# Performance work log

Hardware: AMD Instinct MI355X
Metric: run time of the kernel (lower is better)

The kernel has to match this reference:

```python
import jax, jax.numpy as jnp
import numpy as np

B, L, H, D, TXT = 128, 512, 336, 256, 768
K, S, EMB = 16, 4, 128
H_SCALE = 0.15
EPS, ITERS = 0.05, 30
ALPHA, BETA = 1.0, 0.5
GW, TAU = 0.5, 0.07
LMB_MSE, LMB_COT, LMB_DELTA, LMB_ENT, LMB_TV = 1.0, 0.1, 0.1, 0.01, 0.01


def setup_inputs() -> dict:
    key = jax.random.key(0)
    ks = jax.random.split(key, 12)
    def xav(k, shape):
        return jax.random.normal(k, shape, jnp.float32) / np.sqrt(shape[0]).astype(np.float32)
    inp = {}
    inp['y_res'] = jax.random.normal(ks[0], (B, H, D), jnp.float32)
    inp['text_emb'] = jax.random.normal(ks[1], (B, TXT), jnp.float32)
    inp['enc_out'] = jax.random.normal(ks[2], (B, L, D), jnp.float32)
    inp['y_future'] = jax.random.normal(ks[3], (B, H, D), jnp.float32)
    inp['perm'] = jax.random.permutation(ks[4], EMB)
    inp['W_t2k'] = xav(ks[5], (TXT, K * (3 + S))); inp['b_t2k'] = jnp.zeros((K * (3 + S),), jnp.float32)
    inp['W_kemb'] = xav(ks[6], (H, EMB)); inp['b_kemb'] = jnp.zeros((EMB,), jnp.float32)
    inp['W_tir'] = xav(ks[7], (1, D)); inp['b_tir'] = jnp.zeros((D,), jnp.float32)
    inp['var_proj'] = jnp.ones((D,), jnp.float32)
    inp['W_g1'] = xav(ks[8], (2 * D + TXT, 512)); inp['b_g1'] = jnp.zeros((512,), jnp.float32)
    inp['W_g2'] = xav(ks[9], (512, D)); inp['b_g2'] = jnp.zeros((D,), jnp.float32)
    inp['W_fp'] = xav(ks[10], (3 * D, EMB)); inp['b_fp'] = jnp.zeros((EMB,), jnp.float32)
    return inp


def _text2kernels(text_emb, W, b):
    # text -> K temporal kernels: mixture of S shape bases with learned mu/sigma/amp
    raw = (text_emb @ W + b).reshape(-1, K, 3 + S)
    mu = jax.nn.sigmoid(raw[..., 0])                       # [B,K] center in [0,1]
    sig = jax.nn.softplus(raw[..., 1]) * H_SCALE + 1e-3     # [B,K] width
    amp = jax.nn.softplus(raw[..., 2])                      # [B,K]
    shape_w = jax.nn.softmax(raw[..., 3:], axis=-1)         # [B,K,S]
    t = (jnp.arange(H, dtype=text_emb.dtype) + 0.5) / H     # [H]
    z = (t[None, None, :] - mu[..., None]) / sig[..., None]  # [B,K,H]
    az = jnp.abs(z)
    in_supp = (az <= 1.0).astype(z.dtype)
    basis = jnp.stack([
        jnp.exp(-0.5 * z * z),
        jnp.exp(-az),
        jnp.maximum(1.0 - az, 0.0),
        0.5 * (1.0 + jnp.cos(jnp.pi * jnp.clip(z, -1.0, 1.0))) * in_supp,
    ], axis=-1)                                             # [B,K,H,S]
    kappa = amp[..., None] * jnp.einsum('bkhs,bks->bkh', basis, shape_w)
    return kappa, mu, shape_w


def _future_proj(y, W, b):
    # concat(y, first diff, second diff) -> linear, in_dim = 3*D
    d1 = jnp.diff(y, axis=1, prepend=y[:, :1])
    d2 = jnp.diff(d1, axis=1, prepend=d1[:, :1])
    return jnp.concatenate([y, d1, d2], axis=-1) @ W + b    # [B,H,EMB]


def _l2n(x):
    return x / (jnp.linalg.norm(x, axis=-1, keepdims=True) + 1e-8)


def _causal_cost(k_emb, f_pos, mu):
    cossim = jnp.einsum('bkd,bhd->bkh', _l2n(k_emb), _l2n(f_pos))
    t = (jnp.arange(H, dtype=k_emb.dtype) + 0.5) / H
    causal = jnp.maximum(mu[:, :, None] - t[None, None, :], 0.0)  # effect-before-cause penalty
    return ALPHA * (1.0 - cossim) + BETA * causal            # [B,K,H]


def _sinkhorn(C, r, c):
    Kmat = jnp.exp(-C / EPS)
    def body(i, uv):
        u, v = uv
        u = r / (jnp.einsum('bkh,bh->bk', Kmat, v) + 1e-9)
        v = c / (jnp.einsum('bkh,bk->bh', Kmat, u) + 1e-9)
        return (u, v)
    u, v = jax.lax.fori_loop(0, ITERS, body, (jnp.ones_like(r), jnp.ones_like(c)))
    return u[:, :, None] * Kmat * v[:, None, :]              # [B,K,H]


def _delta_contrastive(k_emb, f_pos, Pi, negatives):
    w = Pi / (jnp.sum(Pi, axis=-1, keepdims=True) + 1e-9)    # transport-weighted aggregation
    kn = _l2n(k_emb)
    def sim(f):
        return jnp.einsum('bkd,bkd->bk', kn, _l2n(jnp.einsum('bkh,bhd->bkd', w, f)))
    logits = jnp.stack([sim(f_pos)] + [sim(f) for f in negatives], axis=-1) / TAU  # [B,K,1+neg]
    return -jnp.mean(jax.nn.log_softmax(logits, axis=-1)[..., 0])


def reference(y_res, text_emb, enc_out, y_future, perm, W_t2k, b_t2k, W_kemb, b_kemb,
              W_tir, b_tir, var_proj, W_g1, b_g1, W_g2, b_g2, W_fp, b_fp):
    # --- text-induced response ---
    kappa, mu, shape_w = _text2kernels(text_emb, W_t2k, b_t2k)   # [B,K,H]
    y_tir_scalar = kappa.sum(axis=1)                             # [B,H]
    # --- gated fusion ---
    y_tir = (y_tir_scalar[..., None] @ W_tir + b_tir) * var_proj[None, None, :]  # [B,H,D]
    ts_global = enc_out.mean(axis=1)                             # [B,D]
    gate_in = jnp.concatenate([ts_global, text_emb, jnp.broadcast_to(var_proj[None, :], (y_res.shape[0], D))], axis=-1)
    gate = jax.nn.sigmoid(jax.nn.relu(gate_in @ W_g1 + b_g1) @ W_g2 + b_g2)[:, None, :]  # [B,1,D]
    y_hat = y_res + GW * gate * (y_tir - y_res)
    # --- aux losses ---
    k_emb = kappa @ W_kemb + b_kemb                              # [B,K,EMB]
    f_pos = _future_proj(y_future, W_fp, b_fp)                   # [B,H,EMB]
    C = _causal_cost(k_emb, f_pos, mu)
    r = jax.lax.stop_gradient(kappa.sum(-1) + 1e-6)
    r = r / r.sum(axis=-1, keepdims=True)
    c = jnp.full((C.shape[0], C.shape[2]), 1.0 / C.shape[2], C.dtype)
    Pi = _sinkhorn(C, r, c)
    shift = max(1, H // 6)
    f_neg1 = jnp.roll(f_pos, shift, axis=1)
    f_neg2 = f_pos[..., perm]
    loss_delta = _delta_contrastive(k_emb, f_pos, Pi, [f_neg1, f_neg2])
    loss_cot = jnp.mean(jnp.sum(C * Pi, axis=(1, 2)))
    sw = jnp.maximum(shape_w, 1e-8)
    loss_ent = -jnp.mean(jnp.sum(sw * jnp.log(sw), axis=-1))
    loss_tv = jnp.mean(jnp.abs(mu[:, 1:] - mu[:, :-1]))
    loss_mse = jnp.mean((y_hat - y_future) ** 2)
    return (LMB_MSE * loss_mse + LMB_COT * loss_cot + LMB_DELTA * loss_delta
            + LMB_ENT * loss_ent + LMB_TV * loss_tv)
```

## Files before the change

### kernel.cpp

```cpp
#include <hip/hip_runtime.h>
#include <math.h>

#define Bn   128
#define Ln   512
#define Hn   336
#define Dn   256
#define TXTn 768
#define Kn   16
#define EMBn 128
#define SHIFT 56
#define MSEB 1024
#define FROWS 48
#define FTILES 7
#define ASTRIDE 776

typedef __attribute__((ext_vector_type(8))) short short8;
typedef __attribute__((ext_vector_type(4))) float floatx4;

__device__ __forceinline__ float softplusf(float x){
  return fmaxf(x, 0.f) + log1pf(expf(-fabsf(x)));
}
__device__ __forceinline__ unsigned short f2bf(float x){
  unsigned int u = __float_as_uint(x);
  unsigned int r = (u + 0x7fffu + ((u >> 16) & 1u)) >> 16;
  return (unsigned short)r;
}
__device__ __forceinline__ float rcpf(float x){ return __builtin_amdgcn_rcpf(x); }
__device__ __forceinline__ float wsum(float x){
  x += __shfl_xor(x, 1);  x += __shfl_xor(x, 2);  x += __shfl_xor(x, 4);
  x += __shfl_xor(x, 8);  x += __shfl_xor(x, 16); x += __shfl_xor(x, 32);
  return x;
}

__global__ __launch_bounds__(256) void k_fused1(
    const float* __restrict__ text, const float* __restrict__ W, const float* __restrict__ bb,
    float* __restrict__ mu_o, float* __restrict__ kapT, float* __restrict__ rr_o,
    float* __restrict__ ytirs, float* __restrict__ part_ent, float* __restrict__ part_tv){
  int b = blockIdx.x, t = threadIdx.x;
  __shared__ float kapS[Kn*Hn];
  __shared__ float musL[Kn], sigL[Kn], ampL[Kn], shwL[Kn*4], entS[Kn], rrS[Kn];
  __shared__ float red[256];
  __shared__ float comb[112];
  __shared__ float totS;
  {
    int o = t & 127, half = t >> 7;
    if (o < 112){
      const float* tb = text + (size_t)b*TXTn + half*384;
      const float* Wb = W + (size_t)half*384*112 + o;
      float a0=0.f, a1=0.f, a2=0.f, a3=0.f;
      for (int i = 0; i < 384; i += 4){
        float4 x = *(const float4*)(tb + i);
        a0 += x.x*Wb[(i+0)*112]; a1 += x.y*Wb[(i+1)*112];
        a2 += x.z*Wb[(i+2)*112]; a3 += x.w*Wb[(i+3)*112];
      }
      red[half*112 + o] = (a0 + a1) + (a2 + a3);
    }
  }
  __syncthreads();
  if (t < 112) comb[t] = red[t] + red[112 + t] + bb[t];
  __syncthreads();
  if (t < Kn){
    float r0 = comb[t*7+0], r1 = comb[t*7+1], r2 = comb[t*7+2];
    float mu  = 1.f/(1.f+expf(-r0));
    float sig = softplusf(r1)*0.15f + 1e-3f;
    float amp = softplusf(r2);
    float s0 = comb[t*7+3], s1 = comb[t*7+4], s2 = comb[t*7+5], s3 = comb[t*7+6];
    float m = fmaxf(fmaxf(s0,s1), fmaxf(s2,s3));
    float e0 = expf(s0-m), e1 = expf(s1-m), e2 = expf(s2-m), e3 = expf(s3-m);
    float inv = 1.f/(e0+e1+e2+e3);
    float w0 = e0*inv, w1 = e1*inv, w2 = e2*inv, w3 = e3*inv;
    musL[t] = mu; sigL[t] = sig; ampL[t] = amp;
    shwL[t*4+0] = w0; shwL[t*4+1] = w1; shwL[t*4+2] = w2; shwL[t*4+3] = w3;
    mu_o[b*Kn + t] = mu;
    float ent = 0.f, sw;
    sw = fmaxf(w0,1e-8f); ent += sw*logf(sw);
    sw = fmaxf(w1,1e-8f); ent += sw*logf(sw);
    sw = fmaxf(w2,1e-8f); ent += sw*logf(sw);
    sw = fmaxf(w3,1e-8f); ent += sw*logf(sw);
    entS[t] = ent;
  }
  __syncthreads();
  for (int p = t; p < Kn*Hn; p += 256){
    int k = p/Hn, h = p - k*Hn;
    float mu = musL[k], sig = sigL[k], amp = ampL[k];
    float w0 = shwL[k*4+0], w1 = shwL[k*4+1], w2 = shwL[k*4+2], w3 = shwL[k*4+3];
    float tt = (h + 0.5f)/(float)Hn;
    float z  = (tt - mu)/sig;
    float az = fabsf(z);
    float b0 = expf(-0.5f*z*z);
    float b1 = expf(-az);
    float b2 = fmaxf(1.f-az, 0.f);
    float zc = fminf(fmaxf(z,-1.f),1.f);
    float b3 = (az <= 1.f) ? 0.5f*(1.f+cosf(3.14159265358979f*zc)) : 0.f;
    kapS[p] = amp*(w0*b0 + w1*b1 + w2*b2 + w3*b3);
  }
  __syncthreads();
  for (int q = t; q < Kn*Hn; q += 256){
    int h = q >> 4, k = q & 15;
    kapT[((size_t)b*Hn + h)*Kn + k] = kapS[k*Hn + h];
  }
  {
    int k = t >> 4, j16 = t & 15;
    float s = 0.f;
    for (int h = j16; h < Hn; h += 16) s += kapS[k*Hn + h];
    red[t] = s;
  }
  __syncthreads();
  if (t < Kn){
    float s = 0.f;
    for (int j = 0; j < 16; ++j) s += red[t*16 + j];
    rrS[t] = s + 1e-6f;
  }
  __syncthreads();
  if (t == 0){
    float tot = 0.f, tv = 0.f, es = 0.f;
    for (int k = 0; k < Kn; ++k) tot += rrS[k];
    for (int k = 1; k < Kn; ++k) tv += fabsf(musL[k]-musL[k-1]);
    for (int k = 0; k < Kn; ++k) es += entS[k];
    totS = tot; part_tv[b] = tv; part_ent[b] = es;
  }
  __syncthreads();
  if (t < Kn) rr_o[b*Kn + t] = rrS[t]/totS;
  for (int h = t; h < Hn; h += 256){
    float s = 0.f;
    #pragma unroll
    for (int k = 0; k < Kn; ++k) s += kapS[k*Hn + h];
    ytirs[b*Hn + h] = s;
  }
}

__global__ __launch_bounds__(128) void k_kemb1(const float* __restrict__ kapT,
    const float* __restrict__ W, float* __restrict__ kp){
  int blk = blockIdx.x;
  int b = blk >> 3, oc = blk & 7;
  int e = threadIdx.x;
  float acc[Kn];
  #pragma unroll
  for (int k = 0; k < Kn; ++k) acc[k] = 0.f;
  const float* kb = kapT + (size_t)b*Hn*Kn;
  int h0 = oc*42, h1 = h0 + 42;
  for (int h = h0; h < h1; ++h){
    float wv = W[h*EMBn + e];
    const float4* kr = (const float4*)(kb + h*Kn);
    float4 c0 = kr[0], c1 = kr[1], c2 = kr[2], c3 = kr[3];
    acc[0]  += c0.x*wv; acc[1]  += c0.y*wv; acc[2]  += c0.z*wv; acc[3]  += c0.w*wv;
    acc[4]  += c1.x*wv; acc[5]  += c1.y*wv; acc[6]  += c1.z*wv; acc[7]  += c1.w*wv;
    acc[8]  += c2.x*wv; acc[9]  += c2.y*wv; acc[10] += c2.z*wv; acc[11] += c2.w*wv;
    acc[12] += c3.x*wv; acc[13] += c3.y*wv; acc[14] += c3.z*wv; acc[15] += c3.w*wv;
  }
  float* kpb = kp + ((size_t)blk*Kn)*EMBn + e;
  #pragma unroll
  for (int k = 0; k < Kn; ++k) kpb[(size_t)k*EMBn] = acc[k];
}

__global__ __launch_bounds__(256) void k_kemb2(const float* __restrict__ kp,
    const float* __restrict__ bb, float* __restrict__ kn_o){
  int b = blockIdx.x, t = threadIdx.x;
  __shared__ float kS[Kn*EMBn];
  __shared__ float r2[256];
  __shared__ float invS[Kn];
  for (int j = t; j < Kn*EMBn; j += 256){
    int e = j & 127;
    float s = bb[e];
    const float* p = kp + (size_t)b*8*Kn*EMBn + j;
    #pragma unroll
    for (int oc = 0; oc < 8; ++oc) s += p[(size_t)oc*Kn*EMBn];
    kS[j] = s;
  }
  __syncthreads();
  {
    int k = t & 15, g = t >> 4;
    float s = 0.f;
    for (int e = g; e < EMBn; e += 16){ float v = kS[k*EMBn + e]; s += v*v; }
    r2[g*Kn + k] = s;
  }
  __syncthreads();
  if (t < Kn){
    float s = 0.f;
    for (int g = 0; g < 16; ++g) s += r2[g*Kn + t];
    invS[t] = 1.f/(sqrtf(s) + 1e-8f);
  }
  __syncthreads();
  for (int j = t; j < Kn*EMBn; j += 256)
    kn_o[(size_t)b*Kn*EMBn + j] = kS[j]*invS[j >> 7];
}

__global__ void k_wprep(const float* __restrict__ W, unsigned short* __restrict__ Bsw){
  int tid = blockIdx.x*256 + threadIdx.x;
  int k = tid >> 7, n = tid & 127;
  int kt = k >> 5, kr = k & 31, quad = kr >> 3, j = kr & 7;
  int c = n >> 4, ln = n & 15;
  int lane = quad*16 + ln;
  int dst = ((kt*8 + c)*64 + lane)*8 + j;
  Bsw[dst] = f2bf(W[k*128 + n]);
}

__global__ __launch_bounds__(256) void k_encmean(const float* __restrict__ enc,
                                                 float* __restrict__ psum){
  int blk = blockIdx.x;
  int b = blk >> 3, p = blk & 7;
  int t = threadIdx.x;
  int d4 = t & 63, rg = t >> 6;
  const float4* e4 = (const float4*)(enc + (size_t)b*Ln*Dn);
  float4 s = make_float4(0.f,0.f,0.f,0.f);
  for (int l = p + 8*rg; l < Ln; l += 32){
    float4 v = e4[(size_t)l*64 + d4];
    s.x += v.x; s.y += v.y; s.z += v.z; s.w += v.w;
  }
  __shared__ float4 red[256];
  red[t] = s;
  __syncthreads();
  if (rg == 0){
    float4 o = red[d4];
    #pragma unroll
    for (int r = 1; r < 4; ++r){
      float4 v = red[r*64 + d4];
      o.x += v.x; o.y += v.y; o.z += v.z; o.w += v.w;
    }
    ((float4*)(psum + ((size_t)b*8 + p)*Dn))[d4] = o;
  }
}

__global__ __launch_bounds__(256) void k_gmlp1(const float* __restrict__ psum,
    const float* __restrict__ text, const float* __restrict__ vp,
    const float* __restrict__ W1, float* __restrict__ hidp){
  int bt = blockIdx.x >> 5, hc = (blockIdx.x >> 2) & 7, ks = blockIdx.x & 3;
  int t = threadIdx.x;
  __shared__ float inS[4][320];
  for (int j = t; j < 4*320; j += 256){
    int bi = j / 320, jj = j - bi*320;
    int gi = ks*320 + jj;
    int b = bt*4 + bi;
    float vsl;
    if (gi < Dn){
      float s = 0.f;
      for (int p = 0; p < 8; ++p) s += psum[((size_t)b*8 + p)*Dn + gi];
      vsl = s * (1.f/(float)Ln);
    } else if (gi < Dn + TXTn){
      vsl = text[(size_t)b*TXTn + (gi - Dn)];
    } else {
      vsl = vp[gi - Dn - TXTn];
    }
    inS[bi][jj] = vsl;
  }
  __syncthreads();
  int h = t & 63, bi = t >> 6;
  int hidx = hc*64 + h;
  const float* Wb = W1 + (size_t)(ks*320)*512 + hidx;
  float a0 = 0.f, a1 = 0.f, a2 = 0.f, a3 = 0.f;
  const float4* in4 = (const float4*)inS[bi];
  for (int i = 0; i < 320; i += 4){
    float4 x = in4[i >> 2];
    a0 += x.x*Wb[(size_t)(i+0)*512]; a1 += x.y*Wb[(size_t)(i+1)*512];
    a2 += x.z*Wb[(size_t)(i+2)*512]; a3 += x.w*Wb[(size_t)(i+3)*512];
  }
  hidp[((size_t)ks*Bn + bt*4 + bi)*512 + hidx] = (a0 + a1) + (a2 + a3);
}

__global__ __launch_bounds__(256) void k_gmlp2(const float* __restrict__ hidp,
    const float* __restrict__ b1, const float* __restrict__ W2,
    const float* __restrict__ b2, float* __restrict__ gate_o){
  int bt = blockIdx.x >> 3, dc = blockIdx.x & 7;
  int t = threadIdx.x;
  __shared__ float hS[4][512];
  __shared__ float pS[8][4][32];
  for (int j = t; j < 4*512; j += 256){
    int bi = j >> 9, i = j & 511;
    size_t bidx = (size_t)(bt*4 + bi)*512 + i;
    float s = hidp[bidx] + hidp[(size_t)Bn*512 + bidx]
            + hidp[(size_t)2*Bn*512 + bidx] + hidp[(size_t)3*Bn*512 + bidx];
    hS[bi][i] = fmaxf(s + b1[i], 0.f);
  }
  __syncthreads();
  {
    int dl = t & 31, ig = t >> 5;
    int d  = dc*32 + dl;
    float a0=0.f, a1=0.f, a2=0.f, a3=0.f;
    int i0 = ig*64;
    for (int i = i0; i < i0 + 64; ++i){
      float wv = W2[(size_t)i*Dn + d];
      a0 += hS[0][i]*wv; a1 += hS[1][i]*wv;
      a2 += hS[2][i]*wv; a3 += hS[3][i]*wv;
    }
    pS[ig][0][dl] = a0; pS[ig][1][dl] = a1;
    pS[ig][2][dl] = a2; pS[ig][3][dl] = a3;
  }
  __syncthreads();
  if (t < 128){
    int bi = t >> 5, dl = t & 31;
    float s = 0.f;
    #pragma unroll
    for (int g = 0; g < 8; ++g) s += pS[g][bi][dl];
    s += b2[dc*32 + dl];
    gate_o[(size_t)(bt*4 + bi)*Dn + dc*32 + dl] = 1.f/(1.f + expf(-s));
  }
}

__global__ __launch_bounds__(256) void k_fposm(const float* __restrict__ yf,
    const unsigned short* __restrict__ Bsw, const float* __restrict__ bb,
    float* __restrict__ fpos, float* __restrict__ finv){
  int b = blockIdx.x / FTILES, tile = blockIdx.x % FTILES;
  int t = threadIdx.x;
  int h0 = tile*FROWS;
  __shared__ unsigned short yS[FROWS*ASTRIDE];
  __shared__ float rsq[4][FROWS];
  const float* yb = yf + (size_t)b*Hn*Dn;

  #pragma unroll
  for (int u = 0; u < 12; ++u){
    int unit = t + 256*u;
    int r = unit >> 6, d4 = unit & 63;
    int h = h0 + r;
    int hm1 = h-1 < 0 ? 0 : h-1;
    int hm2 = h-2 < 0 ? 0 : h-2;
    float4 y   = *(const float4*)(yb + (size_t)h  *Dn + d4*4);
    float4 ym1 = *(const float4*)(yb + (size_t)hm1*Dn + d4*4);
    float4 ym2 = *(const float4*)(yb + (size_t)hm2*Dn + d4*4);
    float4 d1 = make_float4(y.x-ym1.x, y.y-ym1.y, y.z-ym1.z, y.w-ym1.w);
    float4 d2 = make_float4(y.x-2.f*ym1.x+ym2.x, y.y-2.f*ym1.y+ym2.y,
                            y.z-2.f*ym1.z+ym2.z, y.w-2.f*ym1.w+ym2.w);
    union { unsigned short u16[4]; uint2 v; } p;
    unsigned short* base = &yS[r*ASTRIDE + d4*4];
    p.u16[0]=f2bf(y.x);  p.u16[1]=f2bf(y.y);  p.u16[2]=f2bf(y.z);  p.u16[3]=f2bf(y.w);
    *(uint2*)(base)        = p.v;
    p.u16[0]=f2bf(d1.x); p.u16[1]=f2bf(d1.y); p.u16[2]=f2bf(d1.z); p.u16[3]=f2bf(d1.w);
    *(uint2*)(base + 256)  = p.v;
    p.u16[0]=f2bf(d2.x); p.u16[1]=f2bf(d2.y); p.u16[2]=f2bf(d2.z); p.u16[3]=f2bf(d2.w);
    *(uint2*)(base + 512)  = p.v;
  }
  __syncthreads();

  int wv   = __builtin_amdgcn_readfirstlane(t >> 6);
  int lane = t & 63, quad = lane >> 4, ln = lane & 15;
  int c0 = wv*2;
  floatx4 acc[3][2];
  #pragma unroll
  for (int i = 0; i < 3; ++i){
    acc[i][0] = (floatx4){0.f,0.f,0.f,0.f};
    acc[i][1] = (floatx4){0.f,0.f,0.f,0.f};
  }
  #pragma unroll
  for (int kt = 0; kt < 24; ++kt){
    int aoff = kt*32 + quad*8;
    short8 a0 = *(const short8*)&yS[( 0 + ln)*ASTRIDE + aoff];
    short8 a1 = *(const short8*)&yS[(16 + ln)*ASTRIDE + aoff];
    short8 a2 = *(const short8*)&yS[(32 + ln)*ASTRIDE + aoff];
    short8 b0 = *(const short8*)&Bsw[((kt*8 + c0  )*64 + lane)*8];
    short8 b1 = *(const short8*)&Bsw[((kt*8 + c0+1)*64 + lane)*8];
    acc[0][0] = __builtin_amdgcn_mfma_f32_16x16x32_bf16(a0, b0, acc[0][0], 0, 0, 0);
    acc[0][1] = __builtin_amdgcn_mfma_f32_16x16x32_bf16(a0, b1, acc[0][1], 0, 0, 0);
    acc[1][0] = __builtin_amdgcn_mfma_f32_16x16x32_bf16(a1, b0, acc[1][0], 0, 0, 0);
    acc[1][1] = __builtin_amdgcn_mfma_f32_16x16x32_bf16(a1, b1, acc[1][1], 0, 0, 0);
    acc[2][0] = __builtin_amdgcn_mfma_f32_16x16x32_bf16(a2, b0, acc[2][0], 0, 0, 0);
    acc[2][1] = __builtin_amdgcn_mfma_f32_16x16x32_bf16(a2, b1, acc[2][1], 0, 0, 0);
  }

  float bias0 = bb[c0*16 + ln], bias1 = bb[(c0+1)*16 + ln];
  #pragma unroll
  for (int rt = 0; rt < 3; ++rt){
    #pragma unroll
    for (int reg = 0; reg < 4; ++reg){
      int lrow = rt*16 + quad*4 + reg;
      size_t row = (size_t)b*Hn + h0 + lrow;
      float v0 = acc[rt][0][reg] + bias0;
      float v1 = acc[rt][1][reg] + bias1;
      fpos[row*EMBn + c0*16 + ln]     = v0;
      fpos[row*EMBn + (c0+1)*16 + ln] = v1;
      float sq = v0*v0 + v1*v1;
      sq += __shfl_xor(sq, 1); sq += __shfl_xor(sq, 2);
      sq += __shfl_xor(sq, 4); sq += __shfl_xor(sq, 8);
      if (ln == 0) rsq[wv][lrow] = sq;
    }
  }
  __syncthreads();
  if (t < FROWS){
    float s = rsq[0][t] + rsq[1][t] + rsq[2][t] + rsq[3][t];
    finv[(size_t)b*Hn + h0 + t] = 1.f/(sqrtf(s) + 1e-8f);
  }
}

__global__ void k_mse(const float* __restrict__ yres, const float* __restrict__ yfut,
                      const float* __restrict__ gate, const float* __restrict__ ytirs,
                      const float* __restrict__ Wt, const float* __restrict__ bt,
                      const float* __restrict__ vp, float* __restrict__ part_mse){
  const long long total = (long long)Bn*Hn*Dn;
  long long tid = blockIdx.x*(long long)blockDim.x + threadIdx.x;
  long long nth = gridDim.x*(long long)blockDim.x;
  float part = 0.f;
  for (long long i4 = tid; i4*4 < total; i4 += nth){
    long long base = i4*4;
    int b = (int)(base/((long long)Hn*Dn));
    int rem = (int)(base - (long long)b*Hn*Dn);
    int h = rem/Dn, d = rem - h*Dn;
    float4 yr = *(const float4*)(yres + base);
    float4 yv = *(const float4*)(yfut + base);
    float4 g  = *(const float4*)(gate + (size_t)b*Dn + d);
    float4 wt = *(const float4*)(Wt + d);
    float4 bv = *(const float4*)(bt + d);
    float4 vv = *(const float4*)(vp + d);
    float ys = ytirs[b*Hn + h];
    float yt, yh, e;
    yt = (ys*wt.x + bv.x)*vv.x; yh = yr.x + 0.5f*g.x*(yt-yr.x); e = yh-yv.x; part += e*e;
    yt = (ys*wt.y + bv.y)*vv.y; yh = yr.y + 0.5f*g.y*(yt-yr.y); e = yh-yv.y; part += e*e;
    yt = (ys*wt.z + bv.z)*vv.z; yh = yr.z + 0.5f*g.z*(yt-yr.z); e = yh-yv.z; part += e*e;
    yt = (ys*wt.w + bv.w)*vv.w; yh = yr.w + 0.5f*g.w*(yt-yr.w); e = yh-yv.w; part += e*e;
  }
  __shared__ float red[256];
  red[threadIdx.x] = part; __syncthreads();
  for (int s = 128; s > 0; s >>= 1){
    if (threadIdx.x < s) red[threadIdx.x] += red[threadIdx.x + s];
    __syncthreads();
  }
  if (threadIdx.x == 0) part_mse[blockIdx.x] = red[0];
}

__global__ __launch_bounds__(256) void k_cost(const float* __restrict__ kn,
    const float* __restrict__ fpos, const float* __restrict__ finv,
    const float* __restrict__ mu_i, float* __restrict__ Km_g){
  int b = blockIdx.x >> 2, q = blockIdx.x & 3;
  int t = threadIdx.x;
  __shared__ float knS[Kn*132];
  __shared__ float musS[Kn];
  for (int j = t; j < Kn*EMBn; j += 256){
    int k = j >> 7, e = j & 127;
    knS[k*132 + e] = kn[(size_t)b*Kn*EMBn + j];
  }
  if (t < Kn) musS[t] = mu_i[b*Kn + t];
  __syncthreads();
  const int H0 = q*84;
  for (int p = t; p < Kn*84; p += 256){
    int k = p & 15, h = H0 + (p >> 4);
    const float4* f4 = (const float4*)(fpos + ((size_t)b*Hn + h)*EMBn);
    const float4* k4 = (const float4*)(knS + k*132);
    float s = 0.f;
    #pragma unroll 8
    for (int i = 0; i < EMBn/4; ++i){
      float4 a = k4[i], f = f4[i];
      s += a.x*f.x + a.y*f.y + a.z*f.z + a.w*f.w;
    }
    float cs = s*finv[b*Hn + h];
    float th = (h + 0.5f)/(float)Hn;
    float c  = (1.f - cs) + 0.5f*fmaxf(musS[k] - th, 0.f);
    Km_g[(size_t)b*Kn*Hn + k*Hn + h] = expf(-20.f*c);
  }
}

__global__ __launch_bounds__(64) void k_sink1w(const float* __restrict__ rr,
    float* KmwT, float* __restrict__ part_cot){
  int b = blockIdx.x, l = threadIdx.x;
  float* Kb = KmwT + (size_t)b*Kn*Hn;
  int ks = ((l&1)<<3) | ((l&2)<<1) | ((l&4)>>1) | ((l&8)>>3);
  float km[16][6];
  #pragma unroll
  for (int m = 0; m < 16; ++m){
    const float* rowp = Kb + (size_t)(ks ^ m)*Hn;
    #pragma unroll
    for (int i = 0; i < 6; ++i){
      int h = 64*i + l;
      km[m][i] = (h < Hn) ? rowp[h] : 0.f;
    }
  }
  float rrl = rr[b*Kn + ks];
  float v[6];
  #pragma unroll
  for (int i = 0; i < 6; ++i) v[i] = 1.f;
  float w[16];
  for (int it = 0; it < 30; ++it){
    float p[16];
    #pragma unroll
    for (int m = 0; m < 16; ++m){
      float a = km[m][0]*v[0] + km[m][1]*v[1] + km[m][2]*v[2];
      float c = km[m][3]*v[3] + km[m][4]*v[4] + km[m][5]*v[5];
      p[m] = a + c;
    }
    #pragma unroll
    for (int m = 0; m < 8; ++m) p[m] += __shfl_xor(p[m+8], 1);
    #pragma unroll
    for (int m = 0; m < 4; ++m) p[m] += __shfl_xor(p[m+4], 2);
    #pragma unroll
    for (int m = 0; m < 2; ++m) p[m] += __shfl_xor(p[m+2], 4);
    p[0] += __shfl_xor(p[1], 8);
    p[0] += __shfl_xor(p[0], 16);
    p[0] += __shfl_xor(p[0], 32);
    float ul = rrl * rcpf(p[0] + 1e-9f);
    w[0] = ul;
    w[1] = __shfl_xor(w[0], 8);
    w[2] = __shfl_xor(w[0], 4); w[3] = __shfl_xor(w[1], 4);
    #pragma unroll
    for (int j = 0; j < 4; ++j) w[4+j] = __shfl_xor(w[j], 2);
    #pragma unroll
    for (int j = 0; j < 8; ++j) w[8+j] = __shfl_xor(w[j], 1);
    #pragma unroll
    for (int i = 0; i < 6; ++i){
      float s0 = 0.f, s1 = 0.f;
      #pragma unroll
      for (int m = 0; m < 8; ++m){ s0 += km[m][i]*w[m]; s1 += km[m+8][i]*w[m+8]; }
      v[i] = (1.f/(float)Hn) * rcpf(s0 + s1 + 1e-9f);
    }
  }
  float q[16];
  #pragma unroll
  for (int m = 0; m < 16; ++m){
    float a = km[m][0]*v[0] + km[m][1]*v[1] + km[m][2]*v[2];
    float c = km[m][3]*v[3] + km[m][4]*v[4] + km[m][5]*v[5];
    q[m] = a + c;
  }
  #pragma unroll
  for (int m = 0; m < 8; ++m) q[m] += __shfl_xor(q[m+8], 1);
  #pragma unroll
  for (int m = 0; m < 4; ++m) q[m] += __shfl_xor(q[m+4], 2);
  #pragma unroll
  for (int m = 0; m < 2; ++m) q[m] += __shfl_xor(q[m+2], 4);
  q[0] += __shfl_xor(q[1], 8);
  q[0] += __shfl_xor(q[0], 16);
  q[0] += __shfl_xor(q[0], 32);
  float tt[16];
  tt[0] = q[0];
  tt[1] = __shfl_xor(tt[0], 8);
  tt[2] = __shfl_xor(tt[0], 4); tt[3] = __shfl_xor(tt[1], 4);
  #pragma unroll
  for (int j = 0; j < 4; ++j) tt[4+j] = __shfl_xor(tt[j], 2);
  #pragma unroll
  for (int j = 0; j < 8; ++j) tt[8+j] = __shfl_xor(tt[j], 1);
  float cot = 0.f;
  #pragma unroll
  for (int m = 0; m < 16; ++m){
    float rsinv = rcpf(w[m]*tt[m] + 1e-9f);
    float* rowp = Kb + (size_t)(ks ^ m)*Hn;
    #pragma unroll
    for (int i = 0; i < 6; ++i){
      int h = 64*i + l;
      if (h < Hn){
        float Pi = w[m]*km[m][i]*v[i];
        cot += (-0.05f)*logf(km[m][i])*Pi;
        rowp[h] = Pi*rsinv;
      }
    }
  }
  cot = wsum(cot);
  if (l == 0) part_cot[b] = cot;
}

__global__ __launch_bounds__(256) void k_agg(const float* __restrict__ kn,
    const float* __restrict__ fpos, const float* __restrict__ wT,
    const int* __restrict__ perm, float* __restrict__ part_del4){
  int b = blockIdx.x >> 2, kg = blockIdx.x & 3;
  int t = threadIdx.x;
  __shared__ float wTl[Hn*4];
  __shared__ float apH[2][4*EMBn];
  __shared__ float a1H[2][4*EMBn];
  __shared__ int permS[EMBn];
  __shared__ float redW[4];
  if (t < EMBn) permS[t] = perm[t];
  for (int j = t; j < 4*Hn; j += 256){
    int k = j & 3, h = j >> 2;
    wTl[h*4 + k] = wT[(size_t)b*Kn*Hn + (size_t)(kg*4 + k)*Hn + h];
  }
  __syncthreads();

  {
    int e = t & 127, jh = t >> 7;
    float ap[4], a1[4];
    #pragma unroll
    for (int j = 0; j < 4; ++j){ ap[j] = 0.f; a1[j] = 0.f; }
    const float* fb = fpos + (size_t)b*Hn*EMBn + e;
    int hh0 = jh*168, hh1 = hh0 + 168;
    for (int h = hh0; h < hh1; ++h){
      float fv = fb[(size_t)h*EMBn];
      int h1 = h + SHIFT; if (h1 >= Hn) h1 -= Hn;
      float4 wA = *(const float4*)&wTl[h *4];
      float4 wB = *(const float4*)&wTl[h1*4];
      ap[0] += wA.x*fv; ap[1] += wA.y*fv; ap[2] += wA.z*fv; ap[3] += wA.w*fv;
      a1[0] += wB.x*fv; a1[1] += wB.y*fv; a1[2] += wB.z*fv; a1[3] += wB.w*fv;
    }
    #pragma unroll
    for (int j = 0; j < 4; ++j){
      apH[jh][j*EMBn + e] = ap[j];
      a1H[jh][j*EMBn + e] = a1[j];
    }
  }
  __syncthreads();
  for (int j = t; j < 4*EMBn; j += 256){
    apH[0][j] += apH[1][j];
    a1H[0][j] += a1H[1][j];
  }
  __syncthreads();

  int wave = t >> 6, lane = t & 63;
  {
    int kl = wave;
    int k  = kg*4 + kl;
    float sp = 0.f, s1 = 0.f, s2 = 0.f, np = 0.f, n1 = 0.f;
    for (int e = lane; e < EMBn; e += 64){
      float kne = kn[((size_t)b*Kn + k)*EMBn + e];
      float a  = apH[0][kl*EMBn + e];
      float c1 = a1H[0][kl*EMBn + e];
      sp += kne*a; s1 += kne*c1;
      s2 += kne*apH[0][kl*EMBn + permS[e]];
      np += a*a; n1 += c1*c1;
    }
    for (int o = 32; o; o >>= 1){
      sp += __shfl_down(sp, o); s1 += __shfl_down(s1, o); s2 += __shfl_down(s2, o);
      np += __shfl_down(np, o); n1 += __shfl_down(n1, o);
    }
    if (lane == 0){
      float ip  = 1.f/(sqrtf(np) + 1e-8f);
      float i1v = 1.f/(sqrtf(n1) + 1e-8f);
      const float ti = 1.f/0.07f;
      float l0 = sp*ip*ti, l1 = s1*i1v*ti, l2 = s2*ip*ti;
      float m = fmaxf(l0, fmaxf(l1, l2));
      float lse = m + logf(expf(l0-m) + expf(l1-m) + expf(l2-m));
      redW[wave] = lse - l0;
    }
  }
  __syncthreads();
  if (t == 0) part_del4[(size_t)b*4 + kg] = redW[0] + redW[1] + redW[2] + redW[3];
}

__global__ void k_final(const float* __restrict__ part_mse, const float* __restrict__ part_cot,
                        const float* __restrict__ part_del4, const float* __restrict__ part_ent,
                        const float* __restrict__ part_tv, float* __restrict__ out){
  int t = threadIdx.x;
  __shared__ double sred[256];
  double m = 0.0;
  for (int i = t; i < MSEB; i += 256) m += (double)part_mse[i];
  double o4 = 0.0;
  if (t < Bn){
    double del = (double)part_del4[4*t] + (double)part_del4[4*t + 1]
               + (double)part_del4[4*t + 2] + (double)part_del4[4*t + 3];
    o4 = 0.1*(double)part_cot[t] + (0.1/(double)Kn)*del
       - (0.01/(double)Kn)*(double)part_ent[t] + (0.01/(double)(Kn-1))*(double)part_tv[t];
  }
  sred[t] = m/((double)Bn*Hn*Dn) + o4/(double)Bn;
  __syncthreads();
  for (int s = 128; s > 0; s >>= 1){ if (t < s) sred[t] += sred[t+s]; __syncthreads(); }
  if (t == 0) out[0] = (float)sred[0];
}

extern "C" void kernel_launch(void* const* d_in, const int* in_sizes, int n_in,
                              void* d_out, int out_size, void* d_ws, size_t ws_size,
                              hipStream_t stream) {
  const float* y_res  = (const float*)d_in[0];
  const float* text   = (const float*)d_in[1];
  const float* enc    = (const float*)d_in[2];
  const float* yfut   = (const float*)d_in[3];
  const int*   perm   = (const int*)  d_in[4];
  const float* W_t2k  = (const float*)d_in[5];
  const float* b_t2k  = (const float*)d_in[6];
  const float* W_kemb = (const float*)d_in[7];
  const float* b_kemb = (const float*)d_in[8];
  const float* W_tir  = (const float*)d_in[9];
  const float* b_tir  = (const float*)d_in[10];
  const float* vproj  = (const float*)d_in[11];
  const float* W_g1   = (const float*)d_in[12];
  const float* b_g1   = (const float*)d_in[13];
  const float* W_g2   = (const float*)d_in[14];
  const float* b_g2   = (const float*)d_in[15];
  const float* W_fp   = (const float*)d_in[16];
  const float* b_fp   = (const float*)d_in[17];

  float* F = (float*)d_ws;
  float* mu_w   = F;
  float* rr_w   = F + 2048;
  float* ytr_w  = F + 4096;
  float* kapT_w = F + 47104;
  float* kn_w   = F + 735232;
  float* gate_w = F + 997376;
  float* fp_w   = F + 1030144;
  float* fi_w   = F + 6535168;
  float* pmse_w = F + 6578176;
  float* pcot_w = F + 6579200;
  float* pent_w = F + 6579456;
  float* ptv_w  = F + 6579584;
  unsigned short* Bsw_w = (unsigned short*)kapT_w;
  float* KmwT_w = kapT_w;
  float* kp_w   = fp_w;
  float* psum_w = fp_w;
  float* hidp_w = fp_w + 262144;
  float* pdel4_w = gate_w;

  k_fused1 <<<Bn, 256, 0, stream>>>(text, W_t2k, b_t2k, mu_w, kapT_w, rr_w, ytr_w, pent_w, ptv_w);
  k_kemb1  <<<Bn*8, 128, 0, stream>>>(kapT_w, W_kemb, kp_w);
  k_kemb2  <<<Bn, 256, 0, stream>>>(kp_w, b_kemb, kn_w);
  k_wprep  <<<384, 256, 0, stream>>>(W_fp, Bsw_w);
  k_encmean<<<Bn*8, 256, 0, stream>>>(enc, psum_w);
  k_gmlp1  <<<1024, 256, 0, stream>>>(psum_w, text, vproj, W_g1, hidp_w);
  k_gmlp2  <<<256, 256, 0, stream>>>(hidp_w, b_g1, W_g2, b_g2, gate_w);
  k_fposm  <<<Bn*FTILES, 256, 0, stream>>>(yfut, Bsw_w, b_fp, fp_w, fi_w);
  k_mse    <<<MSEB, 256, 0, stream>>>(y_res, yfut, gate_w, ytr_w, W_tir, b_tir, vproj, pmse_w);
  k_cost   <<<Bn*4, 256, 0, stream>>>(kn_w, fp_w, fi_w, mu_w, KmwT_w);
  k_sink1w <<<Bn, 64, 0, stream>>>(rr_w, KmwT_w, pcot_w);
  k_agg    <<<Bn*4, 256, 0, stream>>>(kn_w, fp_w, KmwT_w, perm, pdel4_w);
  k_final  <<<1, 256, 0, stream>>>(pmse_w, pcot_w, pdel4_w, pent_w, ptv_w, (float*)d_out);
}
```

Measured before the change: 356.9 us.

## Split Sinkhorn iterations across two wavefronts per batch with LDS reduction

The Sinkhorn kernel now uses 128 threads per batch instead of 64. Each thread holds three H-columns of the kernel matrix instead of six. Row sums are combined across the two wavefronts through shared memory with barriers each iteration. This halves per-thread serial FMA work and register pressure and uses more CUs. In exchange it adds two block barriers per iteration.

```diff
diff --git a/kernel.cpp b/kernel.cpp
--- a/kernel.cpp
+++ b/kernel.cpp
@@ -445,34 +445,32 @@
   }
 }
 
-__global__ __launch_bounds__(64) void k_sink1w(const float* __restrict__ rr,
+__global__ __launch_bounds__(128) void k_sink1w(const float* __restrict__ rr,
     float* KmwT, float* __restrict__ part_cot){
-  int b = blockIdx.x, l = threadIdx.x;
+  int b = blockIdx.x, t = threadIdx.x;
+  int l = t & 63;
   float* Kb = KmwT + (size_t)b*Kn*Hn;
   int ks = ((l&1)<<3) | ((l&2)<<1) | ((l&4)>>1) | ((l&8)>>3);
-  float km[16][6];
+  __shared__ float ws[128];
+  float km[16][3];
   #pragma unroll
   for (int m = 0; m < 16; ++m){
     const float* rowp = Kb + (size_t)(ks ^ m)*Hn;
     #pragma unroll
-    for (int i = 0; i < 6; ++i){
-      int h = 64*i + l;
-      km[m][i] = (h < Hn) ? rowp[h] : 0.f;
+    for (int c = 0; c < 3; ++c){
+      int h = 128*c + t;
+      km[m][c] = (h < Hn) ? rowp[h] : 0.f;
     }
   }
   float rrl = rr[b*Kn + ks];
-  float v[6];
-  #pragma unroll
-  for (int i = 0; i < 6; ++i) v[i] = 1.f;
+  float v[3];
+  v[0] = 1.f; v[1] = 1.f; v[2] = 1.f;
   float w[16];
   for (int it = 0; it < 30; ++it){
     float p[16];
     #pragma unroll
-    for (int m = 0; m < 16; ++m){
-      float a = km[m][0]*v[0] + km[m][1]*v[1] + km[m][2]*v[2];
-      float c = km[m][3]*v[3] + km[m][4]*v[4] + km[m][5]*v[5];
-      p[m] = a + c;
-    }
+    for (int m = 0; m < 16; ++m)
+      p[m] = km[m][0]*v[0] + km[m][1]*v[1] + km[m][2]*v[2];
     #pragma unroll
     for (int m = 0; m < 8; ++m) p[m] += __shfl_xor(p[m+8], 1);
     #pragma unroll
@@ -482,7 +480,11 @@
     p[0] += __shfl_xor(p[1], 8);
     p[0] += __shfl_xor(p[0], 16);
     p[0] += __shfl_xor(p[0], 32);
-    float ul = rrl * rcpf(p[0] + 1e-9f);
+    ws[t] = p[0];
+    __syncthreads();
+    float ptot = ws[l] + ws[64 + l];
+    __syncthreads();
+    float ul = rrl * rcpf(ptot + 1e-9f);
     w[0] = ul;
     w[1] = __shfl_xor(w[0], 8);
     w[2] = __shfl_xor(w[0], 4); w[3] = __shfl_xor(w[1], 4);
@@ -491,20 +493,17 @@
     #pragma unroll
     for (int j = 0; j < 8; ++j) w[8+j] = __shfl_xor(w[j], 1);
     #pragma unroll
-    for (int i = 0; i < 6; ++i){
+    for (int c = 0; c < 3; ++c){
       float s0 = 0.f, s1 = 0.f;
       #pragma unroll
-      for (int m = 0; m < 8; ++m){ s0 += km[m][i]*w[m]; s1 += km[m+8][i]*w[m+8]; }
-      v[i] = (1.f/(float)Hn) * rcpf(s0 + s1 + 1e-9f);
+      for (int m = 0; m < 8; ++m){ s0 += km[m][c]*w[m]; s1 += km[m+8][c]*w[m+8]; }
+      v[c] = (1.f/(float)Hn) * rcpf(s0 + s1 + 1e-9f);
     }
   }
   float q[16];
   #pragma unroll
-  for (int m = 0; m < 16; ++m){
-    float a = km[m][0]*v[0] + km[m][1]*v[1] + km[m][2]*v[2];
-    float c = km[m][3]*v[3] + km[m][4]*v[4] + km[m][5]*v[5];
-    q[m] = a + c;
-  }
+  for (int m = 0; m < 16; ++m)
+    q[m] = km[m][0]*v[0] + km[m][1]*v[1] + km[m][2]*v[2];
   #pragma unroll
   for (int m = 0; m < 8; ++m) q[m] += __shfl_xor(q[m+8], 1);
   #pragma unroll
@@ -514,8 +513,12 @@
   q[0] += __shfl_xor(q[1], 8);
   q[0] += __shfl_xor(q[0], 16);
   q[0] += __shfl_xor(q[0], 32);
+  ws[t] = q[0];
+  __syncthreads();
+  float qtot = ws[l] + ws[64 + l];
+  __syncthreads();
   float tt[16];
-  tt[0] = q[0];
+  tt[0] = qtot;
   tt[1] = __shfl_xor(tt[0], 8);
   tt[2] = __shfl_xor(tt[0], 4); tt[3] = __shfl_xor(tt[1], 4);
   #pragma unroll
@@ -528,17 +531,19 @@
     float rsinv = rcpf(w[m]*tt[m] + 1e-9f);
     float* rowp = Kb + (size_t)(ks ^ m)*Hn;
     #pragma unroll
-    for (int i = 0; i < 6; ++i){
-      int h = 64*i + l;
+    for (int c = 0; c < 3; ++c){
+      int h = 128*c + t;
       if (h < Hn){
-        float Pi = w[m]*km[m][i]*v[i];
-        cot += (-0.05f)*logf(km[m][i])*Pi;
+        float Pi = w[m]*km[m][c]*v[c];
+        cot += (-0.05f)*logf(km[m][c])*Pi;
         rowp[h] = Pi*rsinv;
       }
     }
   }
   cot = wsum(cot);
-  if (l == 0) part_cot[b] = cot;
+  ws[t] = cot;
+  __syncthreads();
+  if (t == 0) part_cot[b] = ws[0] + ws[64];
 }
 
 __global__ __launch_bounds__(256) void k_agg(const float* __restrict__ kn,
@@ -689,7 +694,7 @@
   k_fposm  <<<Bn*FTILES, 256, 0, stream>>>(yfut, Bsw_w, b_fp, fp_w, fi_w);
   k_mse    <<<MSEB, 256, 0, stream>>>(y_res, yfut, gate_w, ytr_w, W_tir, b_tir, vproj, pmse_w);
   k_cost   <<<Bn*4, 256, 0, stream>>>(kn_w, fp_w, fi_w, mu_w, KmwT_w);
-  k_sink1w <<<Bn, 64, 0, stream>>>(rr_w, KmwT_w, pcot_w);
+  k_sink1w <<<Bn, 128, 0, stream>>>(rr_w, KmwT_w, pcot_w);
   k_agg    <<<Bn*4, 256, 0, stream>>>(kn_w, fp_w, KmwT_w, perm, pdel4_w);
   k_final  <<<1, 256, 0, stream>>>(pmse_w, pcot_w, pdel4_w, pent_w, ptv_w, (float*)d_out);
 }
```

New measurement: 346.0 us. 1.03x faster.
